# Kernel tuning notes

Hardware: AMD Instinct MI355X
Metric: run time of the kernel (lower is better)

The kernel has to match this reference:

```python
import jax, jax.numpy as jnp
import numpy as np

T = 1024
V = 512
K_BINS = jnp.array([1, 2, 3, 4, 5, 6, 7, 8, 12, 16, 24, 32, 48, 64, 96, 128], dtype=jnp.int32)
SPLIT_T = T // 2                      # int(T * 0.5)
CW = max(4, T // 20)                  # crossfade width = 51
FADE_START = SPLIT_T - CW // 2        # 487
FADE_END = SPLIT_T + CW // 2          # 537


def _early_weight():
    t = jnp.arange(T, dtype=jnp.float32)
    fade = 1.0 - (t - FADE_START) / (FADE_END - FADE_START)
    ew = jnp.where(t < FADE_START, 1.0, jnp.where(t < FADE_END, fade, 0.0))
    return ew.reshape(1, T, 1)


def setup_inputs() -> dict:
    key = jax.random.key(0)
    k = jax.random.split(key, 5)
    B = 64
    return {
        "x": jax.random.normal(k[0], (B, T, V), dtype=jnp.float32),
        "g_early_real": jax.random.normal(k[1], (V, 16), dtype=jnp.float32) * 0.1,
        "g_early_imag": jax.random.normal(k[2], (V, 16), dtype=jnp.float32) * 0.1,
        "g_late_real": jax.random.normal(k[3], (V, 16), dtype=jnp.float32) * 0.1,
        "g_late_imag": jax.random.normal(k[4], (V, 16), dtype=jnp.float32) * 0.1,
    }


def reference(x, g_early_real, g_early_imag, g_late_real, g_late_imag):
    # x: [B, T, V] real. rfft along time.
    X = jnp.fft.rfft(x, n=T, axis=1)              # [B, F, V] complex, F = T//2+1
    xb = X[:, K_BINS, :]                          # [B, K, V]
    # complex gain (1 + gr + i*gi), broadcast [1, K, V]
    g_e = (g_early_real + 1j * g_early_imag).T[None, :, :]
    g_l = (g_late_real + 1j * g_late_imag).T[None, :, :]
    Y_e = X.at[:, K_BINS, :].set(xb * (1.0 + g_e))
    Y_l = X.at[:, K_BINS, :].set(xb * (1.0 + g_l))
    y_early = jnp.fft.irfft(Y_e, n=T, axis=1)     # [B, T, V]
    y_late = jnp.fft.irfft(Y_l, n=T, axis=1)
    ew = _early_weight()
    return ew * y_early + (1.0 - ew) * y_late
```

## Files before the change

### kernel.cpp

```cpp
#include <hip/hip_runtime.h>
#include <math.h>

#define T_LEN 1024
#define VV 512
#define VVh 256
#define BB 64
#define NB 16
#define ANG_STEP 0.006135923151542565f
#define FADE_S 487
#define FADE_E 537
#define ATL 64

typedef float v2f __attribute__((ext_vector_type(2)));

__device__ constexpr int KB[NB] = {1,2,3,4,5,6,7,8,12,16,24,32,48,64,96,128};

template<int TLEN>
__global__ __launch_bounds__(256, 2) void k_dft_partial(const float* __restrict__ x,
                                                        float* __restrict__ xpart,
                                                        int tc_count) {
    const int b   = blockIdx.x;
    const int tc  = blockIdx.y;
    const int tid = threadIdx.x;
    const int t0  = tc * TLEN;

    __shared__ float2 tab[TLEN][NB];
    for (int i = tid; i < TLEN * NB; i += 256) {
        int t = i >> 4, j = i & 15;
        int idx = (KB[j] * (t0 + t)) & (T_LEN - 1);
        float ss, cc; sincosf(ANG_STEP * (float)idx, &ss, &cc);
        tab[t][j] = make_float2(cc, ss);
    }
    __syncthreads();

    float xr0[NB], xi0[NB], xr1[NB], xi1[NB];
#pragma unroll
    for (int j = 0; j < NB; ++j) { xr0[j] = xi0[j] = xr1[j] = xi1[j] = 0.0f; }

    const float2* xrd = (const float2*)(x + ((size_t)b * T_LEN + t0) * VV) + tid;

#define DFT_T(TT, AV)                                           \
    do {                                                        \
        _Pragma("unroll")                                       \
        for (int j = 0; j < NB; ++j) {                          \
            float2 cs = tab[(TT)][j];                           \
            xr0[j] = fmaf((AV).x, cs.x, xr0[j]);                \
            xi0[j] = fmaf(-(AV).x, cs.y, xi0[j]);               \
            xr1[j] = fmaf((AV).y, cs.x, xr1[j]);                \
            xi1[j] = fmaf(-(AV).y, cs.y, xi1[j]);               \
        }                                                       \
    } while (0)

    float2 a0 = xrd[(size_t)0 * VVh];
    float2 a1 = xrd[(size_t)1 * VVh];
    float2 a2 = xrd[(size_t)2 * VVh];
    float2 a3 = xrd[(size_t)3 * VVh];
    float2 a4 = xrd[(size_t)4 * VVh];
    float2 a5 = xrd[(size_t)5 * VVh];
    float2 a6 = xrd[(size_t)6 * VVh];
    float2 a7 = xrd[(size_t)7 * VVh];
#pragma unroll 1
    for (int t = 0; t < TLEN - 8; t += 8) {
        float2 b0 = xrd[(size_t)(t +  8) * VVh];
        float2 b1 = xrd[(size_t)(t +  9) * VVh];
        float2 b2 = xrd[(size_t)(t + 10) * VVh];
        float2 b3 = xrd[(size_t)(t + 11) * VVh];
        float2 b4 = xrd[(size_t)(t + 12) * VVh];
        float2 b5 = xrd[(size_t)(t + 13) * VVh];
        float2 b6 = xrd[(size_t)(t + 14) * VVh];
        float2 b7 = xrd[(size_t)(t + 15) * VVh];
        DFT_T(t + 0, a0); DFT_T(t + 1, a1); DFT_T(t + 2, a2); DFT_T(t + 3, a3);
        DFT_T(t + 4, a4); DFT_T(t + 5, a5); DFT_T(t + 6, a6); DFT_T(t + 7, a7);
        a0 = b0; a1 = b1; a2 = b2; a3 = b3;
        a4 = b4; a5 = b5; a6 = b6; a7 = b7;
    }
    {
        const int t = TLEN - 8;
        DFT_T(t + 0, a0); DFT_T(t + 1, a1); DFT_T(t + 2, a2); DFT_T(t + 3, a3);
        DFT_T(t + 4, a4); DFT_T(t + 5, a5); DFT_T(t + 6, a6); DFT_T(t + 7, a7);
    }
#undef DFT_T

    float2* o = (float2*)(xpart + (size_t)(b * tc_count + tc) * 32 * VV) + tid;
#pragma unroll
    for (int j = 0; j < NB; ++j) {
        o[(size_t)j        * VVh] = make_float2(xr0[j], xr1[j]);
        o[(size_t)(NB + j) * VVh] = make_float2(xi0[j], xi1[j]);
    }
}

__global__ __launch_bounds__(256) void k_combine(const float* __restrict__ xpart,
                                                 const float* __restrict__ ger,
                                                 const float* __restrict__ gei,
                                                 const float* __restrict__ glr,
                                                 const float* __restrict__ gli,
                                                 float* __restrict__ H, int tc_count) {
    const int b   = blockIdx.x;
    const int j   = blockIdx.y;
    const int tid = threadIdx.x;
    const int v0  = tid * 2;

    float re0 = 0.f, re1 = 0.f, im0 = 0.f, im1 = 0.f;
#pragma unroll 8
    for (int tc = 0; tc < tc_count; ++tc) {
        const float2* p = (const float2*)(xpart + (size_t)(b * tc_count + tc) * 32 * VV) + tid;
        float2 a  = p[(size_t)j        * VVh];
        float2 bb = p[(size_t)(NB + j) * VVh];
        re0 += a.x;  re1 += a.y;
        im0 += bb.x; im1 += bb.y;
    }

    const float scale = 2.0f / (float)T_LEN;
    float er0 = ger[v0 * NB + j],       ei0 = gei[v0 * NB + j];
    float lr0 = glr[v0 * NB + j],       li0 = gli[v0 * NB + j];
    float er1 = ger[(v0 + 1) * NB + j], ei1 = gei[(v0 + 1) * NB + j];
    float lr1 = glr[(v0 + 1) * NB + j], li1 = gli[(v0 + 1) * NB + j];

    float here0 = (re0 * er0 - im0 * ei0) * scale;
    float heim0 = (re0 * ei0 + im0 * er0) * scale;
    float hlre0 = (re0 * lr0 - im0 * li0) * scale;
    float hlim0 = (re0 * li0 + im0 * lr0) * scale;
    float here1 = (re1 * er1 - im1 * ei1) * scale;
    float heim1 = (re1 * ei1 + im1 * er1) * scale;
    float hlre1 = (re1 * lr1 - im1 * li1) * scale;
    float hlim1 = (re1 * li1 + im1 * lr1) * scale;

    float2* o = (float2*)(H + (size_t)b * 64 * VV) + tid;
    o[(size_t)j        * VVh] = make_float2(here0, here1);
    o[(size_t)(16 + j) * VVh] = make_float2(-heim0, -heim1);
    o[(size_t)(32 + j) * VVh] = make_float2(hlre0, hlre1);
    o[(size_t)(48 + j) * VVh] = make_float2(-hlim0, -hlim1);
}

__global__ __launch_bounds__(256, 2) void k_apply(const float* __restrict__ x,
                                                  const float* __restrict__ H,
                                                  float* __restrict__ out) {
    const int b    = blockIdx.x;
    const int tile = blockIdx.y;
    const int tid  = threadIdx.x;
    const int t0   = tile * ATL;
    const int qo   = (tile < 8) ? 0 : 32;

    __shared__ float2 tab[ATL][NB];
    for (int i = tid; i < ATL * NB; i += 256) {
        int t = i >> 4, j = i & 15;
        int idx = (KB[j] * (t0 + t)) & (T_LEN - 1);
        float ss, cc; sincosf(ANG_STEP * (float)idx, &ss, &cc);
        tab[t][j] = make_float2(cc, ss);
    }

    float hr0[NB], hi0[NB], hr1[NB], hi1[NB];
    const float2* hp = (const float2*)(H + (size_t)b * 64 * VV) + tid;
#pragma unroll
    for (int j = 0; j < NB; ++j) {
        float2 a  = hp[(size_t)(qo + j)      * VVh]; hr0[j] = a.x;  hr1[j] = a.y;
        float2 bq = hp[(size_t)(qo + 16 + j) * VVh]; hi0[j] = bq.x; hi1[j] = bq.y;
    }
    __syncthreads();

    const float2* xrd = (const float2*)(x + ((size_t)b * T_LEN + t0) * VV) + tid;
    v2f*          ow  = (v2f*)(out + ((size_t)b * T_LEN + t0) * VV) + tid;

#define APPLY_T(TT, AV)                                         \
    do {                                                        \
        float s0 = 0.f, s1 = 0.f;                               \
        _Pragma("unroll")                                       \
        for (int j = 0; j < NB; ++j) {                          \
            float2 cs = tab[(TT)][j];                           \
            s0 = fmaf(hr0[j], cs.x, s0);                        \
            s0 = fmaf(hi0[j], cs.y, s0);                        \
            s1 = fmaf(hr1[j], cs.x, s1);                        \
            s1 = fmaf(hi1[j], cs.y, s1);                        \
        }                                                       \
        v2f ov; ov.x = (AV).x + s0; ov.y = (AV).y + s1;         \
        __builtin_nontemporal_store(ov,                         \
            &ow[(size_t)(TT) * VVh]);                           \
    } while (0)

    float2 a0 = xrd[(size_t)0 * VVh];
    float2 a1 = xrd[(size_t)1 * VVh];
    float2 a2 = xrd[(size_t)2 * VVh];
    float2 a3 = xrd[(size_t)3 * VVh];
    float2 a4 = xrd[(size_t)4 * VVh];
    float2 a5 = xrd[(size_t)5 * VVh];
    float2 a6 = xrd[(size_t)6 * VVh];
    float2 a7 = xrd[(size_t)7 * VVh];
#pragma unroll 1
    for (int t = 0; t < ATL - 8; t += 8) {
        float2 b0 = xrd[(size_t)(t +  8) * VVh];
        float2 b1 = xrd[(size_t)(t +  9) * VVh];
        float2 b2 = xrd[(size_t)(t + 10) * VVh];
        float2 b3 = xrd[(size_t)(t + 11) * VVh];
        float2 b4 = xrd[(size_t)(t + 12) * VVh];
        float2 b5 = xrd[(size_t)(t + 13) * VVh];
        float2 b6 = xrd[(size_t)(t + 14) * VVh];
        float2 b7 = xrd[(size_t)(t + 15) * VVh];
        APPLY_T(t + 0, a0); APPLY_T(t + 1, a1); APPLY_T(t + 2, a2); APPLY_T(t + 3, a3);
        APPLY_T(t + 4, a4); APPLY_T(t + 5, a5); APPLY_T(t + 6, a6); APPLY_T(t + 7, a7);
        a0 = b0; a1 = b1; a2 = b2; a3 = b3;
        a4 = b4; a5 = b5; a6 = b6; a7 = b7;
    }
    {
        const int t = ATL - 8;
        APPLY_T(t + 0, a0); APPLY_T(t + 1, a1); APPLY_T(t + 2, a2); APPLY_T(t + 3, a3);
        APPLY_T(t + 4, a4); APPLY_T(t + 5, a5); APPLY_T(t + 6, a6); APPLY_T(t + 7, a7);
    }
#undef APPLY_T
}

__global__ __launch_bounds__(512) void k_fixup(const float* __restrict__ x,
                                               const float* __restrict__ H,
                                               float* __restrict__ out) {
    const int b   = blockIdx.x;
    const int tz  = blockIdx.y;
    const int tid = threadIdx.x;
    const int ts  = tz ? 512 : FADE_S;
    const int te  = tz ? FADE_E : 512;
    const int nt  = te - ts;

    __shared__ float2 tab[32][NB];
    for (int i = tid; i < nt * NB; i += 512) {
        int t = i >> 4, j = i & 15;
        int idx = (KB[j] * (ts + t)) & (T_LEN - 1);
        float ss, cc; sincosf(ANG_STEP * (float)idx, &ss, &cc);
        tab[t][j] = make_float2(cc, ss);
    }

    float er[NB], ei[NB], lr[NB], li[NB];
    const float* hp = H + (size_t)b * 64 * VV + tid;
#pragma unroll
    for (int j = 0; j < NB; ++j) {
        er[j] = hp[(size_t)j        * VV];
        ei[j] = hp[(size_t)(16 + j) * VV];
        lr[j] = hp[(size_t)(32 + j) * VV];
        li[j] = hp[(size_t)(48 + j) * VV];
    }
    __syncthreads();

    const float* xrd = x + ((size_t)b * T_LEN + ts) * VV + tid;
    float*       ow  = out + ((size_t)b * T_LEN + ts) * VV + tid;

    for (int t = 0; t < nt; ++t) {
        float av = xrd[(size_t)t * VV];
        const int tg = ts + t;
        float se = 0.f, sl = 0.f;
#pragma unroll
        for (int j = 0; j < NB; ++j) {
            float2 cs = tab[t][j];
            se = fmaf(er[j], cs.x, se); se = fmaf(ei[j], cs.y, se);
            sl = fmaf(lr[j], cs.x, sl); sl = fmaf(li[j], cs.y, sl);
        }
        float w = 1.0f - (float)(tg - FADE_S) * (1.0f / 50.0f);
        ow[(size_t)t * VV] = av + fmaf(w, se - sl, sl);
    }
}

extern "C" void kernel_launch(void* const* d_in, const int* in_sizes, int n_in,
                              void* d_out, int out_size, void* d_ws, size_t ws_size,
                              hipStream_t stream) {
    (void)in_sizes; (void)n_in; (void)out_size;
    const float* x   = (const float*)d_in[0];
    const float* ger = (const float*)d_in[1];
    const float* gei = (const float*)d_in[2];
    const float* glr = (const float*)d_in[3];
    const float* gli = (const float*)d_in[4];
    float* out = (float*)d_out;

    const size_t hflts = (size_t)BB * 64 * VV;
    int TC;
    if (((size_t)BB * 8 * 32 * VV + hflts) * sizeof(float) <= ws_size)  TC = 8;
    else                                                                TC = 4;

    float* xpart = (float*)d_ws;
    float* H     = xpart + (size_t)BB * TC * 32 * VV;

    if (TC == 8) k_dft_partial<128><<<dim3(BB, 8), 256, 0, stream>>>(x, xpart, 8);
    else         k_dft_partial<256><<<dim3(BB, 4), 256, 0, stream>>>(x, xpart, 4);

    k_combine<<<dim3(BB, NB), 256, 0, stream>>>(xpart, ger, gei, glr, gli, H, TC);
    k_apply<<<dim3(BB, 16), 256, 0, stream>>>(x, H, out);
    k_fixup<<<dim3(BB, 2), 512, 0, stream>>>(x, H, out);
}
```

Before: 115.4 us.

## Widen per-thread column work to float4 in DFT and apply kernels

Each thread now handles four adjacent columns using float4 loads and stores instead of two. In the DFT kernel the block is split into two halves over time, which doubles the number of partial-sum slices that the combine kernel reduces. The apply kernel drops to 128 threads per block with four columns per thread. The aim is to reuse each shared-memory twiddle load across more FMAs and to issue wider memory accesses. The cost is double the accumulator registers, which may lower occupancy or cause spills, plus more partial-sum traffic to combine.

```diff
diff --git a/kernel.cpp b/kernel.cpp
--- a/kernel.cpp
+++ b/kernel.cpp
@@ -3,7 +3,6 @@
 
 #define T_LEN 1024
 #define VV 512
-#define VVh 256
 #define BB 64
 #define NB 16
 #define ANG_STEP 0.006135923151542565f
@@ -11,18 +10,21 @@
 #define FADE_E 537
 #define ATL 64
 
-typedef float v2f __attribute__((ext_vector_type(2)));
+typedef float v4f __attribute__((ext_vector_type(4)));
 
 __device__ constexpr int KB[NB] = {1,2,3,4,5,6,7,8,12,16,24,32,48,64,96,128};
 
 template<int TLEN>
 __global__ __launch_bounds__(256, 2) void k_dft_partial(const float* __restrict__ x,
                                                         float* __restrict__ xpart,
-                                                        int tc_count) {
-    const int b   = blockIdx.x;
-    const int tc  = blockIdx.y;
-    const int tid = threadIdx.x;
-    const int t0  = tc * TLEN;
+                                                        int tcx_count) {
+    const int b    = blockIdx.x;
+    const int tc   = blockIdx.y;
+    const int tid  = threadIdx.x;
+    const int h    = tid >> 7;
+    const int lane = tid & 127;
+    const int t0   = tc * TLEN;
+    const int HT   = TLEN / 2;
 
     __shared__ float2 tab[TLEN][NB];
     for (int i = tid; i < TLEN * NB; i += 256) {
@@ -34,58 +36,57 @@
     __syncthreads();
 
     float xr0[NB], xi0[NB], xr1[NB], xi1[NB];
-#pragma unroll
-    for (int j = 0; j < NB; ++j) { xr0[j] = xi0[j] = xr1[j] = xi1[j] = 0.0f; }
-
-    const float2* xrd = (const float2*)(x + ((size_t)b * T_LEN + t0) * VV) + tid;
+    float xr2[NB], xi2[NB], xr3[NB], xi3[NB];
+#pragma unroll
+    for (int j = 0; j < NB; ++j) {
+        xr0[j] = xi0[j] = xr1[j] = xi1[j] = 0.0f;
+        xr2[j] = xi2[j] = xr3[j] = xi3[j] = 0.0f;
+    }
+
+    const int th0 = h * HT;
+    const float4* xrd = (const float4*)(x + ((size_t)b * T_LEN + t0 + th0) * VV) + lane;
 
 #define DFT_T(TT, AV)                                           \
     do {                                                        \
         _Pragma("unroll")                                       \
         for (int j = 0; j < NB; ++j) {                          \
-            float2 cs = tab[(TT)][j];                           \
+            float2 cs = tab[th0 + (TT)][j];                     \
             xr0[j] = fmaf((AV).x, cs.x, xr0[j]);                \
             xi0[j] = fmaf(-(AV).x, cs.y, xi0[j]);               \
             xr1[j] = fmaf((AV).y, cs.x, xr1[j]);                \
             xi1[j] = fmaf(-(AV).y, cs.y, xi1[j]);               \
+            xr2[j] = fmaf((AV).z, cs.x, xr2[j]);                \
+            xi2[j] = fmaf(-(AV).z, cs.y, xi2[j]);               \
+            xr3[j] = fmaf((AV).w, cs.x, xr3[j]);                \
+            xi3[j] = fmaf(-(AV).w, cs.y, xi3[j]);               \
         }                                                       \
     } while (0)
 
-    float2 a0 = xrd[(size_t)0 * VVh];
-    float2 a1 = xrd[(size_t)1 * VVh];
-    float2 a2 = xrd[(size_t)2 * VVh];
-    float2 a3 = xrd[(size_t)3 * VVh];
-    float2 a4 = xrd[(size_t)4 * VVh];
-    float2 a5 = xrd[(size_t)5 * VVh];
-    float2 a6 = xrd[(size_t)6 * VVh];
-    float2 a7 = xrd[(size_t)7 * VVh];
+    float4 a0 = xrd[(size_t)0 * 128];
+    float4 a1 = xrd[(size_t)1 * 128];
+    float4 a2 = xrd[(size_t)2 * 128];
+    float4 a3 = xrd[(size_t)3 * 128];
 #pragma unroll 1
-    for (int t = 0; t < TLEN - 8; t += 8) {
-        float2 b0 = xrd[(size_t)(t +  8) * VVh];
-        float2 b1 = xrd[(size_t)(t +  9) * VVh];
-        float2 b2 = xrd[(size_t)(t + 10) * VVh];
-        float2 b3 = xrd[(size_t)(t + 11) * VVh];
-        float2 b4 = xrd[(size_t)(t + 12) * VVh];
-        float2 b5 = xrd[(size_t)(t + 13) * VVh];
-        float2 b6 = xrd[(size_t)(t + 14) * VVh];
-        float2 b7 = xrd[(size_t)(t + 15) * VVh];
+    for (int t = 0; t < HT - 4; t += 4) {
+        float4 b0 = xrd[(size_t)(t + 4) * 128];
+        float4 b1 = xrd[(size_t)(t + 5) * 128];
+        float4 b2 = xrd[(size_t)(t + 6) * 128];
+        float4 b3 = xrd[(size_t)(t + 7) * 128];
         DFT_T(t + 0, a0); DFT_T(t + 1, a1); DFT_T(t + 2, a2); DFT_T(t + 3, a3);
-        DFT_T(t + 4, a4); DFT_T(t + 5, a5); DFT_T(t + 6, a6); DFT_T(t + 7, a7);
         a0 = b0; a1 = b1; a2 = b2; a3 = b3;
-        a4 = b4; a5 = b5; a6 = b6; a7 = b7;
     }
     {
-        const int t = TLEN - 8;
+        const int t = HT - 4;
         DFT_T(t + 0, a0); DFT_T(t + 1, a1); DFT_T(t + 2, a2); DFT_T(t + 3, a3);
-        DFT_T(t + 4, a4); DFT_T(t + 5, a5); DFT_T(t + 6, a6); DFT_T(t + 7, a7);
     }
 #undef DFT_T
 
-    float2* o = (float2*)(xpart + (size_t)(b * tc_count + tc) * 32 * VV) + tid;
-#pragma unroll
-    for (int j = 0; j < NB; ++j) {
-        o[(size_t)j        * VVh] = make_float2(xr0[j], xr1[j]);
-        o[(size_t)(NB + j) * VVh] = make_float2(xi0[j], xi1[j]);
+    const int tcx = tc * 2 + h;
+    float4* o = (float4*)(xpart + (size_t)(b * tcx_count + tcx) * 32 * VV) + lane;
+#pragma unroll
+    for (int j = 0; j < NB; ++j) {
+        o[(size_t)j        * 128] = make_float4(xr0[j], xr1[j], xr2[j], xr3[j]);
+        o[(size_t)(NB + j) * 128] = make_float4(xi0[j], xi1[j], xi2[j], xi3[j]);
     }
 }
 
@@ -104,8 +105,8 @@
 #pragma unroll 8
     for (int tc = 0; tc < tc_count; ++tc) {
         const float2* p = (const float2*)(xpart + (size_t)(b * tc_count + tc) * 32 * VV) + tid;
-        float2 a  = p[(size_t)j        * VVh];
-        float2 bb = p[(size_t)(NB + j) * VVh];
+        float2 a  = p[(size_t)j        * 256];
+        float2 bb = p[(size_t)(NB + j) * 256];
         re0 += a.x;  re1 += a.y;
         im0 += bb.x; im1 += bb.y;
     }
@@ -126,13 +127,13 @@
     float hlim1 = (re1 * li1 + im1 * lr1) * scale;
 
     float2* o = (float2*)(H + (size_t)b * 64 * VV) + tid;
-    o[(size_t)j        * VVh] = make_float2(here0, here1);
-    o[(size_t)(16 + j) * VVh] = make_float2(-heim0, -heim1);
-    o[(size_t)(32 + j) * VVh] = make_float2(hlre0, hlre1);
-    o[(size_t)(48 + j) * VVh] = make_float2(-hlim0, -hlim1);
-}
-
-__global__ __launch_bounds__(256, 2) void k_apply(const float* __restrict__ x,
+    o[(size_t)j        * 256] = make_float2(here0, here1);
+    o[(size_t)(16 + j) * 256] = make_float2(-heim0, -heim1);
+    o[(size_t)(32 + j) * 256] = make_float2(hlre0, hlre1);
+    o[(size_t)(48 + j) * 256] = make_float2(-hlim0, -hlim1);
+}
+
+__global__ __launch_bounds__(128, 2) void k_apply(const float* __restrict__ x,
                                                   const float* __restrict__ H,
                                                   float* __restrict__ out) {
     const int b    = blockIdx.x;
@@ -142,7 +143,7 @@
     const int qo   = (tile < 8) ? 0 : 32;
 
     __shared__ float2 tab[ATL][NB];
-    for (int i = tid; i < ATL * NB; i += 256) {
+    for (int i = tid; i < ATL * NB; i += 128) {
         int t = i >> 4, j = i & 15;
         int idx = (KB[j] * (t0 + t)) & (T_LEN - 1);
         float ss, cc; sincosf(ANG_STEP * (float)idx, &ss, &cc);
@@ -150,20 +151,23 @@
     }
 
     float hr0[NB], hi0[NB], hr1[NB], hi1[NB];
-    const float2* hp = (const float2*)(H + (size_t)b * 64 * VV) + tid;
-#pragma unroll
-    for (int j = 0; j < NB; ++j) {
-        float2 a  = hp[(size_t)(qo + j)      * VVh]; hr0[j] = a.x;  hr1[j] = a.y;
-        float2 bq = hp[(size_t)(qo + 16 + j) * VVh]; hi0[j] = bq.x; hi1[j] = bq.y;
+    float hr2[NB], hi2[NB], hr3[NB], hi3[NB];
+    const float4* hp = (const float4*)(H + (size_t)b * 64 * VV) + tid;
+#pragma unroll
+    for (int j = 0; j < NB; ++j) {
+        float4 a  = hp[(size_t)(qo + j)      * 128];
+        hr0[j] = a.x;  hr1[j] = a.y;  hr2[j] = a.z;  hr3[j] = a.w;
+        float4 bq = hp[(size_t)(qo + 16 + j) * 128];
+        hi0[j] = bq.x; hi1[j] = bq.y; hi2[j] = bq.z; hi3[j] = bq.w;
     }
     __syncthreads();
 
-    const float2* xrd = (const float2*)(x + ((size_t)b * T_LEN + t0) * VV) + tid;
-    v2f*          ow  = (v2f*)(out + ((size_t)b * T_LEN + t0) * VV) + tid;
+    const float4* xrd = (const float4*)(x + ((size_t)b * T_LEN + t0) * VV) + tid;
+    v4f*          ow  = (v4f*)(out + ((size_t)b * T_LEN + t0) * VV) + tid;
 
 #define APPLY_T(TT, AV)                                         \
     do {                                                        \
-        float s0 = 0.f, s1 = 0.f;                               \
+        float s0 = 0.f, s1 = 0.f, s2 = 0.f, s3 = 0.f;           \
         _Pragma("unroll")                                       \
         for (int j = 0; j < NB; ++j) {                          \
             float2 cs = tab[(TT)][j];                           \
@@ -171,39 +175,33 @@
             s0 = fmaf(hi0[j], cs.y, s0);                        \
             s1 = fmaf(hr1[j], cs.x, s1);                        \
             s1 = fmaf(hi1[j], cs.y, s1);                        \
+            s2 = fmaf(hr2[j], cs.x, s2);                        \
+            s2 = fmaf(hi2[j], cs.y, s2);                        \
+            s3 = fmaf(hr3[j], cs.x, s3);                        \
+            s3 = fmaf(hi3[j], cs.y, s3);                        \
         }                                                       \
-        v2f ov; ov.x = (AV).x + s0; ov.y = (AV).y + s1;         \
+        v4f ov; ov.x = (AV).x + s0; ov.y = (AV).y + s1;         \
+        ov.z = (AV).z + s2; ov.w = (AV).w + s3;                 \
         __builtin_nontemporal_store(ov,                         \
-            &ow[(size_t)(TT) * VVh]);                           \
+            &ow[(size_t)(TT) * 128]);                           \
     } while (0)
 
-    float2 a0 = xrd[(size_t)0 * VVh];
-    float2 a1 = xrd[(size_t)1 * VVh];
-    float2 a2 = xrd[(size_t)2 * VVh];
-    float2 a3 = xrd[(size_t)3 * VVh];
-    float2 a4 = xrd[(size_t)4 * VVh];
-    float2 a5 = xrd[(size_t)5 * VVh];
-    float2 a6 = xrd[(size_t)6 * VVh];
-    float2 a7 = xrd[(size_t)7 * VVh];
+    float4 a0 = xrd[(size_t)0 * 128];
+    float4 a1 = xrd[(size_t)1 * 128];
+    float4 a2 = xrd[(size_t)2 * 128];
+    float4 a3 = xrd[(size_t)3 * 128];
 #pragma unroll 1
-    for (int t = 0; t < ATL - 8; t += 8) {
-        float2 b0 = xrd[(size_t)(t +  8) * VVh];
-        float2 b1 = xrd[(size_t)(t +  9) * VVh];
-        float2 b2 = xrd[(size_t)(t + 10) * VVh];
-        float2 b3 = xrd[(size_t)(t + 11) * VVh];
-        float2 b4 = xrd[(size_t)(t + 12) * VVh];
-        float2 b5 = xrd[(size_t)(t + 13) * VVh];
-        float2 b6 = xrd[(size_t)(t + 14) * VVh];
-        float2 b7 = xrd[(size_t)(t + 15) * VVh];
+    for (int t = 0; t < ATL - 4; t += 4) {
+        float4 b0 = xrd[(size_t)(t + 4) * 128];
+        float4 b1 = xrd[(size_t)(t + 5) * 128];
+        float4 b2 = xrd[(size_t)(t + 6) * 128];
+        float4 b3 = xrd[(size_t)(t + 7) * 128];
         APPLY_T(t + 0, a0); APPLY_T(t + 1, a1); APPLY_T(t + 2, a2); APPLY_T(t + 3, a3);
-        APPLY_T(t + 4, a4); APPLY_T(t + 5, a5); APPLY_T(t + 6, a6); APPLY_T(t + 7, a7);
         a0 = b0; a1 = b1; a2 = b2; a3 = b3;
-        a4 = b4; a5 = b5; a6 = b6; a7 = b7;
     }
     {
-        const int t = ATL - 8;
+        const int t = ATL - 4;
         APPLY_T(t + 0, a0); APPLY_T(t + 1, a1); APPLY_T(t + 2, a2); APPLY_T(t + 3, a3);
-        APPLY_T(t + 4, a4); APPLY_T(t + 5, a5); APPLY_T(t + 6, a6); APPLY_T(t + 7, a7);
     }
 #undef APPLY_T
 }
@@ -267,17 +265,17 @@
     float* out = (float*)d_out;
 
     const size_t hflts = (size_t)BB * 64 * VV;
-    int TC;
-    if (((size_t)BB * 8 * 32 * VV + hflts) * sizeof(float) <= ws_size)  TC = 8;
-    else                                                                TC = 4;
+    int tcx;
+    if (((size_t)BB * 16 * 32 * VV + hflts) * sizeof(float) <= ws_size) tcx = 16;
+    else                                                                tcx = 8;
 
     float* xpart = (float*)d_ws;
-    float* H     = xpart + (size_t)BB * TC * 32 * VV;
-
-    if (TC == 8) k_dft_partial<128><<<dim3(BB, 8), 256, 0, stream>>>(x, xpart, 8);
-    else         k_dft_partial<256><<<dim3(BB, 4), 256, 0, stream>>>(x, xpart, 4);
-
-    k_combine<<<dim3(BB, NB), 256, 0, stream>>>(xpart, ger, gei, glr, gli, H, TC);
-    k_apply<<<dim3(BB, 16), 256, 0, stream>>>(x, H, out);
+    float* H     = xpart + (size_t)BB * tcx * 32 * VV;
+
+    if (tcx == 16) k_dft_partial<128><<<dim3(BB, 8), 256, 0, stream>>>(x, xpart, 16);
+    else           k_dft_partial<256><<<dim3(BB, 4), 256, 0, stream>>>(x, xpart, 8);
+
+    k_combine<<<dim3(BB, NB), 256, 0, stream>>>(xpart, ger, gei, glr, gli, H, tcx);
+    k_apply<<<dim3(BB, 16), 128, 0, stream>>>(x, H, out);
     k_fixup<<<dim3(BB, 2), 512, 0, stream>>>(x, H, out);
 }
```

Result: no change. 114.9 us (-0.4%).
